# Optimization experiments

Hardware: AMD Instinct MI355X
Metric: run time of the kernel (lower is better)

The kernel has to match this reference:

```python
import jax, jax.numpy as jnp
import numpy as np

N = 50000      # nodes
E = 400000     # edges (before self-loops)
IN = 256       # in_dim
H = 4          # heads in layer 1
C = 64         # h_dim (per-head channels, layer 1)
OUT = 16       # out_dim (layer 2, 1 head)
NEG_SLOPE = 0.2


def gatv2_layer(x, src, dst, Wl, bl, Wr, br, att, bias, heads, ch, concat, num_nodes):
    # x: [N, F]; src/dst: [E']; Wl/Wr: [F, heads*ch]; att: [heads, ch]
    xl = (x @ Wl + bl).reshape(num_nodes, heads, ch)  # source transform
    xr = (x @ Wr + br).reshape(num_nodes, heads, ch)  # target transform
    m = xl[src] + xr[dst]                              # [E', H, C] gather
    e = jnp.sum(jax.nn.leaky_relu(m, NEG_SLOPE) * att, axis=-1)  # [E', H]
    # segment softmax over incoming edges of each dst node (self-loops ensure non-empty)
    emax = jax.ops.segment_max(e, dst, num_segments=num_nodes)   # [N, H]
    ee = jnp.exp(e - emax[dst])
    denom = jax.ops.segment_sum(ee, dst, num_segments=num_nodes)  # [N, H]
    alpha = ee / (denom[dst] + 1e-16)                              # [E', H]
    out = jax.ops.segment_sum(alpha[..., None] * xl[src], dst, num_segments=num_nodes)  # [N,H,C]
    if concat:
        out = out.reshape(num_nodes, heads * ch)
    else:
        out = out.mean(axis=1)
    return out + bias


def setup_inputs() -> dict:
    key = jax.random.key(0)
    ks = jax.random.split(key, 16)
    s = 0.05
    inp = {
        "x": jax.random.normal(ks[0], (N, IN), jnp.float32),
        "edge_index": jax.random.randint(ks[1], (2, E), 0, N),
        # layer 1 params (in_dim -> heads*h_dim)
        "Wl1": jax.random.normal(ks[2], (IN, H * C), jnp.float32) * s,
        "bl1": jnp.zeros((H * C,), jnp.float32),
        "Wr1": jax.random.normal(ks[3], (IN, H * C), jnp.float32) * s,
        "br1": jnp.zeros((H * C,), jnp.float32),
        "att1": jax.random.normal(ks[4], (H, C), jnp.float32) * s,
        "bias1": jnp.zeros((H * C,), jnp.float32),
        # layer 2 params (heads*h_dim -> out_dim, 1 head)
        "Wl2": jax.random.normal(ks[5], (H * C, OUT), jnp.float32) * s,
        "bl2": jnp.zeros((OUT,), jnp.float32),
        "Wr2": jax.random.normal(ks[6], (H * C, OUT), jnp.float32) * s,
        "br2": jnp.zeros((OUT,), jnp.float32),
        "att2": jax.random.normal(ks[7], (1, OUT), jnp.float32) * s,
        "bias2": jnp.zeros((OUT,), jnp.float32),
    }
    return inp


def reference(x, edge_index, Wl1, bl1, Wr1, br1, att1, bias1, Wl2, bl2, Wr2, br2, att2, bias2):
    # add self loops (PyG GATv2Conv default add_self_loops=True)
    loop = jnp.arange(N, dtype=edge_index.dtype)
    src = jnp.concatenate([edge_index[0], loop])
    dst = jnp.concatenate([edge_index[1], loop])
    h = gatv2_layer(x, src, dst, Wl1, bl1, Wr1, br1, att1, bias1, H, C, True, N)
    h = jnp.tanh(h)
    o = gatv2_layer(h, src, dst, Wl2, bl2, Wr2, br2, att2, bias2, 1, OUT, False, N)
    return o, jax.nn.log_softmax(o, axis=1)
```

## Files before the change

### kernel.cpp

```cpp
#include <hip/hip_runtime.h>

typedef __bf16 bfv8 __attribute__((ext_vector_type(8)));
typedef float f32x4 __attribute__((ext_vector_type(4)));
typedef short shortv8 __attribute__((ext_vector_type(8)));

__device__ __forceinline__ float b2f(unsigned short u) {
  unsigned int v = ((unsigned int)u) << 16;
  float f;
  __builtin_memcpy(&f, &v, 4);
  return f;
}
__device__ __forceinline__ unsigned short f2b(float f) {
  unsigned int u;
  __builtin_memcpy(&u, &f, 4);
  u += 0x7fffu + ((u >> 16) & 1u);
  return (unsigned short)(u >> 16);
}

__global__ void probe_kernel(const unsigned short* __restrict__ x, int* __restrict__ flag) {
  int lane = threadIdx.x;
  int cnt = 0;
  for (int i = lane; i < 4096; i += 64) {
    unsigned int e = (x[i] >> 7) & 0xffu;
    if (e >= 0x86u) cnt++;
  }
#pragma unroll
  for (int off = 1; off < 64; off <<= 1) cnt += __shfl_xor(cnt, off, 64);
  if (lane == 0) *flag = (cnt > 100) ? 1 : 0;
}

__global__ __launch_bounds__(256) void conv_x_kernel(const void* __restrict__ x,
                                                     unsigned short* __restrict__ dst,
                                                     const int* __restrict__ flagp, int n) {
  int i = (blockIdx.x * 256 + threadIdx.x) * 4;
  if (i >= n) return;
  if (*flagp) {
    float4 f = *reinterpret_cast<const float4*>((const float*)x + i);
    ushort4 o;
    o.x = f2b(f.x); o.y = f2b(f.y); o.z = f2b(f.z); o.w = f2b(f.w);
    *reinterpret_cast<ushort4*>(dst + i) = o;
  } else {
    *reinterpret_cast<ushort4*>(dst + i) =
        *reinterpret_cast<const ushort4*>((const unsigned short*)x + i);
  }
}

#define P_TOT 140352
__global__ __launch_bounds__(256) void conv_params_kernel(
    const void* p0, const void* p1, const void* p2, const void* p3,
    const void* p4, const void* p5, const void* p6, const void* p7,
    const void* p8, const void* p9, const void* p10, const void* p11,
    unsigned short* __restrict__ dst, const int* __restrict__ flagp) {
  int i = blockIdx.x * 256 + threadIdx.x;
  if (i >= P_TOT) return;
  const int offs[13] = {0, 65536, 65792, 131328, 131584, 131840, 132096,
                        136192, 136208, 140304, 140320, 140336, P_TOT};
  const void* ptrs[12] = {p0, p1, p2, p3, p4, p5, p6, p7, p8, p9, p10, p11};
  int flag = *flagp;
  int t = 0;
  while (i >= offs[t + 1]) t++;
  int local = i - offs[t];
  unsigned short v;
  if (flag) v = f2b(((const float*)ptrs[t])[local]);
  else v = ((const unsigned short*)ptrs[t])[local];
  dst[i] = v;
}

__global__ __launch_bounds__(256) void transpose_w_kernel(
    const unsigned short* __restrict__ Pc,
    unsigned short* __restrict__ WT1, unsigned short* __restrict__ WT2) {
  int idx = blockIdx.x * 256 + threadIdx.x;
  if (idx < 512 * 256) {
    int n = idx >> 8, k = idx & 255;
    WT1[idx] = (n < 256) ? Pc[0 + k * 256 + n]
                         : Pc[65792 + k * 256 + (n - 256)];
  } else {
    int j = idx - 512 * 256;
    if (j < 32 * 256) {
      int n = j >> 8, k = j & 255;
      WT2[j] = (n < 16) ? Pc[132096 + k * 16 + n]
                        : Pc[136208 + k * 16 + (n - 16)];
    }
  }
}

__global__ __launch_bounds__(256) void gemm1_kernel(
    const unsigned short* __restrict__ X,
    const unsigned short* __restrict__ WT,
    const unsigned short* __restrict__ bl, const unsigned short* __restrict__ br,
    unsigned short* __restrict__ C, int M) {
  __shared__ unsigned short smem[18432];
  const int t = threadIdx.x;
  const int lane = t & 63;
  const int w = t >> 6;
  const int quad = lane >> 4;
  const int l16 = lane & 15;
  const int n_blk = blockIdx.x;
  const int m_base = blockIdx.y * 128 + (w >> 1) * 64;
  const int n_base = n_blk * 128 + (w & 1) * 64;

  const int st_row = t >> 3;
  const int st_seg = t & 7;
  const unsigned short* wt_base =
      WT + ((size_t)(n_blk * 128 + st_row)) * 256 + st_seg * 8;

  f32x4 acc[4][4];
#pragma unroll
  for (int i = 0; i < 4; i++)
#pragma unroll
    for (int j = 0; j < 4; j++) acc[i][j] = (f32x4){0.f, 0.f, 0.f, 0.f};

  shortv8 st[4];
#pragma unroll
  for (int i = 0; i < 4; i++)
    st[i] = *reinterpret_cast<const shortv8*>(wt_base + (size_t)(32 * i) * 256);
#pragma unroll
  for (int i = 0; i < 4; i++) {
    int row = st_row + 32 * i;
    *reinterpret_cast<shortv8*>(smem + row * 64 + ((st_seg ^ (row & 7)) * 8)) = st[i];
  }
  __syncthreads();

#pragma unroll
  for (int c = 0; c < 4; c++) {
    if (c < 3) {
#pragma unroll
      for (int i = 0; i < 4; i++)
        st[i] = *reinterpret_cast<const shortv8*>(wt_base + (size_t)(32 * i) * 256 +
                                                  (c + 1) * 64);
    }
    const unsigned short* bb = smem + (c & 1) * 8192;
#pragma unroll
    for (int sub = 0; sub < 2; sub++) {
      bfv8 a[4], b[4];
      int seg_r = sub * 4 + quad;
#pragma unroll
      for (int i = 0; i < 4; i++) {
        int row = m_base + 16 * i + l16;
        if (row >= M) row = M - 1;
        a[i] = *reinterpret_cast<const bfv8*>(X + (size_t)row * 256 + c * 64 + sub * 32 +
                                              quad * 8);
      }
#pragma unroll
      for (int j = 0; j < 4; j++) {
        int col = (w & 1) * 64 + 16 * j + l16;
        b[j] = *reinterpret_cast<const bfv8*>(bb + col * 64 + ((seg_r ^ (col & 7)) * 8));
      }
#pragma unroll
      for (int i = 0; i < 4; i++)
#pragma unroll
        for (int j = 0; j < 4; j++)
          acc[i][j] = __builtin_amdgcn_mfma_f32_16x16x32_bf16(a[i], b[j], acc[i][j], 0, 0, 0);
    }
    if (c < 3) {
      int buf = (c + 1) & 1;
#pragma unroll
      for (int i = 0; i < 4; i++) {
        int row = st_row + 32 * i;
        *reinterpret_cast<shortv8*>(smem + buf * 8192 + row * 64 +
                                    ((st_seg ^ (row & 7)) * 8)) = st[i];
      }
      __syncthreads();
    }
  }

  __syncthreads();
  unsigned short* lt = smem + w * 4608;
#pragma unroll
  for (int j = 0; j < 4; j++) {
    int col = n_base + 16 * j + l16;
    float bias = (col < 256) ? b2f(bl[col]) : b2f(br[col - 256]);
#pragma unroll
    for (int i = 0; i < 4; i++)
#pragma unroll
      for (int r = 0; r < 4; r++)
        lt[(16 * i + quad * 4 + r) * 72 + 16 * j + l16] = f2b(acc[i][j][r] + bias);
  }
#pragma unroll
  for (int pass = 0; pass < 8; pass++) {
    int row = pass * 8 + (lane >> 3);
    int colg = (lane & 7) * 8;
    shortv8 v = *reinterpret_cast<const shortv8*>(lt + row * 72 + colg);
    int grow = m_base + row;
    if (grow < M)
      *reinterpret_cast<shortv8*>(C + (size_t)grow * 512 + n_base - (w & 1) * 64 +
                                  (w & 1) * 64 + colg) = v;
  }
}

__global__ __launch_bounds__(256) void gemm2_kernel(
    const unsigned short* __restrict__ H, const unsigned short* __restrict__ WT,
    const unsigned short* __restrict__ bl, const unsigned short* __restrict__ br,
    float* __restrict__ C, int M) {
  const int lane = threadIdx.x & 63;
  const int w = threadIdx.x >> 6;
  const int quad = lane >> 4;
  const int l16 = lane & 15;
  const int m_base = blockIdx.x * 256 + w * 64;

  f32x4 acc[4][2];
#pragma unroll
  for (int i = 0; i < 4; i++)
#pragma unroll
    for (int j = 0; j < 2; j++) acc[i][j] = (f32x4){0.f, 0.f, 0.f, 0.f};

#pragma unroll
  for (int k0 = 0; k0 < 256; k0 += 32) {
    bfv8 a[4], b[2];
#pragma unroll
    for (int i = 0; i < 4; i++) {
      int row = m_base + 16 * i + l16;
      if (row >= M) row = M - 1;
      a[i] = *reinterpret_cast<const bfv8*>(H + (size_t)row * 256 + k0 + quad * 8);
    }
#pragma unroll
    for (int j = 0; j < 2; j++) {
      int col = 16 * j + l16;
      b[j] = *reinterpret_cast<const bfv8*>(WT + (size_t)col * 256 + k0 + quad * 8);
    }
#pragma unroll
    for (int i = 0; i < 4; i++)
#pragma unroll
      for (int j = 0; j < 2; j++)
        acc[i][j] = __builtin_amdgcn_mfma_f32_16x16x32_bf16(a[i], b[j], acc[i][j], 0, 0, 0);
  }

#pragma unroll
  for (int j = 0; j < 2; j++) {
    int col = 16 * j + l16;
    float bias = (j == 0) ? b2f(bl[l16]) : b2f(br[l16]);
#pragma unroll
    for (int i = 0; i < 4; i++) {
#pragma unroll
      for (int r = 0; r < 4; r++) {
        int row = m_base + 16 * i + quad * 4 + r;
        if (row < M) C[(size_t)row * 32 + col] = acc[i][j][r] + bias;
      }
    }
  }
}

__global__ __launch_bounds__(256) void count_kernel(const int* __restrict__ ei, int E, int Nn,
                                                    int* __restrict__ cnt) {
  int i = blockIdx.x * 256 + threadIdx.x;
  int total = E + Nn;
  if (i >= total) return;
  int d = (i < E) ? ei[E + i] : (i - E);
  if ((unsigned)d >= (unsigned)Nn) d = 0;
  atomicAdd(&cnt[d], 1);
}

__global__ __launch_bounds__(1024) void scan1_kernel(const int* __restrict__ cnt,
                                                     int* __restrict__ row_start,
                                                     int* __restrict__ blkTot, int Nn) {
  __shared__ int buf[1024];
  int t = threadIdx.x;
  int i = blockIdx.x * 1024 + t;
  int v = (i < Nn) ? cnt[i] : 0;
  buf[t] = v;
  __syncthreads();
  for (int off = 1; off < 1024; off <<= 1) {
    int x = (t >= off) ? buf[t - off] : 0;
    __syncthreads();
    buf[t] += x;
    __syncthreads();
  }
  if (i < Nn) row_start[i] = buf[t] - v;
  if (t == 1023) blkTot[blockIdx.x] = buf[1023];
}

__global__ __launch_bounds__(64) void scan2_kernel(const int* __restrict__ blkTot,
                                                   int* __restrict__ blkOff, int nb,
                                                   int* __restrict__ row_start, int Nn,
                                                   int total) {
  int lane = threadIdx.x;
  int v = (lane < nb) ? blkTot[lane] : 0;
  int s = v;
#pragma unroll
  for (int off = 1; off < 64; off <<= 1) {
    int u = __shfl_up(s, off, 64);
    if (lane >= off) s += u;
  }
  if (lane < nb) blkOff[lane] = s - v;
  if (lane == 0) row_start[Nn] = total;
}

__global__ __launch_bounds__(1024) void scan3_kernel(int* __restrict__ row_start,
                                                     int* __restrict__ cursor,
                                                     const int* __restrict__ blkOff, int Nn) {
  int i = blockIdx.x * 1024 + threadIdx.x;
  if (i < Nn) {
    int val = row_start[i] + blkOff[blockIdx.x];
    row_start[i] = val;
    cursor[i] = val;
  }
}

__global__ __launch_bounds__(256) void fill_kernel(const int* __restrict__ ei, int E, int Nn,
                                                   int* __restrict__ cursor,
                                                   int* __restrict__ csr_src) {
  int i = blockIdx.x * 256 + threadIdx.x;
  int total = E + Nn;
  if (i >= total) return;
  int s, d;
  if (i < E) { s = ei[i]; d = ei[E + i]; } else { s = i - E; d = i - E; }
  if ((unsigned)d >= (unsigned)Nn) d = 0;
  if ((unsigned)s >= (unsigned)Nn) s = 0;
  int pos = atomicAdd(&cursor[d], 1);
  if ((unsigned)pos < (unsigned)total) csr_src[pos] = s;
}

__global__ __launch_bounds__(256) void agg1_kernel(
    const unsigned short* __restrict__ C1,
    const unsigned short* __restrict__ att1,
    const unsigned short* __restrict__ bias1,
    const int* __restrict__ row_start, const int* __restrict__ csr_src,
    unsigned short* __restrict__ H1,
    int Nn, int Etot) {
  int wid = blockIdx.x * 4 + (threadIdx.x >> 6);
  if (wid >= Nn) return;
  int lane = threadIdx.x & 63;
  int c0 = lane * 4;

  ushort4 a4 = *reinterpret_cast<const ushort4*>(att1 + c0);
  float at0 = b2f(a4.x), at1 = b2f(a4.y), at2 = b2f(a4.z), at3 = b2f(a4.w);
  ushort4 r4 = *reinterpret_cast<const ushort4*>(C1 + (size_t)wid * 512 + 256 + c0);
  float xr0 = b2f(r4.x), xr1 = b2f(r4.y), xr2 = b2f(r4.z), xr3 = b2f(r4.w);

  float denom = 0.f, a0 = 0.f, a1 = 0.f, a2 = 0.f, a3 = 0.f;
  int beg = row_start[wid], end = row_start[wid + 1];
  if (beg < 0) beg = 0;
  if (end < beg || end - beg > Etot) end = beg;
  int n = end - beg;

  ushort4 cur0 = make_ushort4(0, 0, 0, 0), cur1 = cur0;
  if (n > 0) {
    int s = csr_src[beg];
    if ((unsigned)s >= (unsigned)Nn) s = 0;
    cur0 = *reinterpret_cast<const ushort4*>(C1 + (size_t)s * 512 + c0);
  }
  if (n > 1) {
    int s = csr_src[beg + 1];
    if ((unsigned)s >= (unsigned)Nn) s = 0;
    cur1 = *reinterpret_cast<const ushort4*>(C1 + (size_t)s * 512 + c0);
  }

#define AGG1_BODY(XV)                                                        \
  {                                                                          \
    float xl0 = b2f(XV.x), xl1 = b2f(XV.y), xl2 = b2f(XV.z), xl3 = b2f(XV.w); \
    float m0 = xl0 + xr0, m1 = xl1 + xr1, m2 = xl2 + xr2, m3 = xl3 + xr3;    \
    float l0 = m0 > 0.f ? m0 : 0.2f * m0;                                    \
    float l1 = m1 > 0.f ? m1 : 0.2f * m1;                                    \
    float l2 = m2 > 0.f ? m2 : 0.2f * m2;                                    \
    float l3 = m3 > 0.f ? m3 : 0.2f * m3;                                    \
    float part = l0 * at0 + l1 * at1 + l2 * at2 + l3 * at3;                  \
    part += __shfl_xor(part, 1, 64);                                         \
    part += __shfl_xor(part, 2, 64);                                         \
    part += __shfl_xor(part, 4, 64);                                         \
    part += __shfl_xor(part, 8, 64);                                         \
    part = fminf(fmaxf(part, -60.f), 60.f);                                  \
    float wgt = __expf(part);                                                \
    denom += wgt;                                                            \
    a0 += wgt * xl0; a1 += wgt * xl1; a2 += wgt * xl2; a3 += wgt * xl3;      \
  }

  int i = 0;
  for (; i + 2 <= n; i += 2) {
    ushort4 nxt0 = cur0, nxt1 = cur1;
    int q0 = beg + i + 2, q1 = beg + i + 3;
    if (q0 < end) {
      int s = csr_src[q0];
      if ((unsigned)s >= (unsigned)Nn) s = 0;
      nxt0 = *reinterpret_cast<const ushort4*>(C1 + (size_t)s * 512 + c0);
    }
    if (q1 < end) {
      int s = csr_src[q1];
      if ((unsigned)s >= (unsigned)Nn) s = 0;
      nxt1 = *reinterpret_cast<const ushort4*>(C1 + (size_t)s * 512 + c0);
    }
    AGG1_BODY(cur0);
    AGG1_BODY(cur1);
    cur0 = nxt0;
    cur1 = nxt1;
  }
  if (i < n) AGG1_BODY(cur0);
#undef AGG1_BODY

  float inv = 1.f / (denom + 1e-16f);
  ushort4 b4 = *reinterpret_cast<const ushort4*>(bias1 + c0);
  float h0 = tanhf(a0 * inv + b2f(b4.x));
  float h1 = tanhf(a1 * inv + b2f(b4.y));
  float h2 = tanhf(a2 * inv + b2f(b4.z));
  float h3 = tanhf(a3 * inv + b2f(b4.w));
  if (!(h0 == h0)) h0 = 0.f;
  if (!(h1 == h1)) h1 = 0.f;
  if (!(h2 == h2)) h2 = 0.f;
  if (!(h3 == h3)) h3 = 0.f;
  ushort4 o4;
  o4.x = f2b(h0); o4.y = f2b(h1); o4.z = f2b(h2); o4.w = f2b(h3);
  *reinterpret_cast<ushort4*>(H1 + (size_t)wid * 256 + c0) = o4;
}

__global__ __launch_bounds__(256) void agg2_kernel(
    const float* __restrict__ C2,
    const unsigned short* __restrict__ att2,
    const unsigned short* __restrict__ bias2,
    const int* __restrict__ row_start, const int* __restrict__ csr_src,
    float* __restrict__ out,
    int Nn, int Etot) {
  int wid = blockIdx.x * 4 + (threadIdx.x >> 6);
  if (wid >= Nn) return;
  int lane = threadIdx.x & 63;
  int g = lane >> 4;
  int c = lane & 15;

  float att = b2f(att2[c]);
  float xr = C2[(size_t)wid * 32 + 16 + c];
  float denom = 0.f, acc = 0.f;
  int beg = row_start[wid], end = row_start[wid + 1];
  if (beg < 0) beg = 0;
  if (end < beg || end - beg > Etot) end = beg;

  int p = beg + g;
  float xl_cur = 0.f;
  if (p < end) {
    int s = csr_src[p];
    if ((unsigned)s >= (unsigned)Nn) s = 0;
    xl_cur = C2[(size_t)s * 32 + c];
  }
  while (p < end) {
    int pn = p + 4;
    float xl_nxt = 0.f;
    if (pn < end) {
      int s = csr_src[pn];
      if ((unsigned)s >= (unsigned)Nn) s = 0;
      xl_nxt = C2[(size_t)s * 32 + c];
    }
    float mm = xl_cur + xr;
    float lr = mm > 0.f ? mm : 0.2f * mm;
    float part = lr * att;
    part += __shfl_xor(part, 1, 64);
    part += __shfl_xor(part, 2, 64);
    part += __shfl_xor(part, 4, 64);
    part += __shfl_xor(part, 8, 64);
    part = fminf(fmaxf(part, -60.f), 60.f);
    float wgt = __expf(part);
    denom += wgt;
    acc += wgt * xl_cur;
    xl_cur = xl_nxt;
    p = pn;
  }
  denom += __shfl_xor(denom, 16, 64);
  denom += __shfl_xor(denom, 32, 64);
  acc += __shfl_xor(acc, 16, 64);
  acc += __shfl_xor(acc, 32, 64);

  float o = acc / (denom + 1e-16f) + b2f(bias2[c]);
  if (!(o == o)) o = 0.f;
  float mx = o;
  mx = fmaxf(mx, __shfl_xor(mx, 1, 64));
  mx = fmaxf(mx, __shfl_xor(mx, 2, 64));
  mx = fmaxf(mx, __shfl_xor(mx, 4, 64));
  mx = fmaxf(mx, __shfl_xor(mx, 8, 64));
  float ex = expf(o - mx);
  float se = ex;
  se += __shfl_xor(se, 1, 64);
  se += __shfl_xor(se, 2, 64);
  se += __shfl_xor(se, 4, 64);
  se += __shfl_xor(se, 8, 64);
  float ls = logf(se);
  if (lane < 16) {
    out[(size_t)wid * 16 + c] = o;
    out[(size_t)Nn * 16 + (size_t)wid * 16 + c] = o - mx - ls;
  }
}

extern "C" void kernel_launch(void* const* d_in, const int* in_sizes, int n_in,
                              void* d_out, int out_size, void* d_ws, size_t ws_size,
                              hipStream_t stream) {
  const void* x_raw = d_in[0];
  const int* ei     = (const int*)d_in[1];

  const int M = in_sizes[0] / 256;
  const int E = in_sizes[1] / 2;
  const int TOT = E + M;
  const int NX = M * 256;

  char* ws = (char*)d_ws;
  size_t off = 0;
  auto alloc = [&](size_t bytes) -> void* {
    void* p = ws + off;
    off = (off + bytes + 255) & ~(size_t)255;
    return p;
  };
  int*            flag   = (int*)alloc(4);
  unsigned short* Pc     = (unsigned short*)alloc((size_t)P_TOT * 2);
  unsigned short* Xc     = (unsigned short*)alloc((size_t)NX * 2);
  unsigned short* WT1    = (unsigned short*)alloc((size_t)512 * 256 * 2);
  unsigned short* WT2    = (unsigned short*)alloc((size_t)32 * 256 * 2);
  int*            cnt    = (int*)alloc((size_t)M * 4);
  int*            cursor = (int*)alloc((size_t)M * 4);
  int*            row_start = (int*)alloc((size_t)(M + 1) * 4);
  int*            csr_src   = (int*)alloc((size_t)TOT * 4);
  int*            blkTot = (int*)alloc(64 * 4);
  int*            blkOff = (int*)alloc(64 * 4);
  float*          C2     = (float*)alloc((size_t)M * 32 * 4);
  unsigned short* C1     = (unsigned short*)alloc((size_t)M * 512 * 2);
  const size_t need = off;
  (void)n_in;
  unsigned short* H1 = Xc;

  if (ws_size < need) {
    hipMemsetAsync(d_out, 0, (size_t)out_size * 4, stream);
    return;
  }

  unsigned short* bl1c   = Pc + 65536;
  unsigned short* br1c   = Pc + 131328;
  unsigned short* att1c  = Pc + 131584;
  unsigned short* bias1c = Pc + 131840;
  unsigned short* bl2c   = Pc + 136192;
  unsigned short* br2c   = Pc + 140304;
  unsigned short* att2c  = Pc + 140320;
  unsigned short* bias2c = Pc + 140336;

  hipMemsetAsync(cnt, 0, (size_t)M * 4, stream);

  probe_kernel<<<1, 64, 0, stream>>>((const unsigned short*)x_raw, flag);
  conv_x_kernel<<<(NX / 4 + 255) / 256, 256, 0, stream>>>(x_raw, Xc, flag, NX);
  conv_params_kernel<<<(P_TOT + 255) / 256, 256, 0, stream>>>(
      d_in[2], d_in[3], d_in[4], d_in[5], d_in[6], d_in[7], d_in[8], d_in[9],
      d_in[10], d_in[11], d_in[12], d_in[13], Pc, flag);

  transpose_w_kernel<<<(512 * 256 + 32 * 256 + 255) / 256, 256, 0, stream>>>(Pc, WT1, WT2);

  dim3 g1(4, (M + 127) / 128);
  gemm1_kernel<<<g1, 256, 0, stream>>>(Xc, WT1, bl1c, br1c, C1, M);

  count_kernel<<<(TOT + 255) / 256, 256, 0, stream>>>(ei, E, M, cnt);
  int nb = (M + 1023) / 1024;
  scan1_kernel<<<nb, 1024, 0, stream>>>(cnt, row_start, blkTot, M);
  scan2_kernel<<<1, 64, 0, stream>>>(blkTot, blkOff, nb, row_start, M, TOT);
  scan3_kernel<<<nb, 1024, 0, stream>>>(row_start, cursor, blkOff, M);
  fill_kernel<<<(TOT + 255) / 256, 256, 0, stream>>>(ei, E, M, cursor, csr_src);

  agg1_kernel<<<(M + 3) / 4, 256, 0, stream>>>(C1, att1c, bias1c, row_start, csr_src,
                                               H1, M, TOT);

  gemm2_kernel<<<(M + 255) / 256, 256, 0, stream>>>(H1, WT2, bl2c, br2c, C2, M);

  agg2_kernel<<<(M + 3) / 4, 256, 0, stream>>>(C2, att2c, bias2c, row_start, csr_src,
                                               (float*)d_out, M, TOT);
}
```

Baseline: 316.0 us.

## Process multiple edges per wavefront in GAT aggregation kernels with wider vector loads

The layer-1 aggregation now splits each wavefront into two halves that handle two edges at once, each lane loading 8 bf16 channels with a 16-byte load. The layer-2 aggregation handles 16 edges per iteration with float4 loads per lane. Both kernels combine partial sums with cross-lane shuffles at the end. The aim is more independent gathers in flight and fewer loop iterations per node, at the cost of dropping the explicit software prefetch, wasting lanes on short neighbour lists, and replacing tanhf with an exp-based formula.

```diff
diff --git a/kernel.cpp b/kernel.cpp
--- a/kernel.cpp
+++ b/kernel.cpp
@@ -3,6 +3,7 @@
 typedef __bf16 bfv8 __attribute__((ext_vector_type(8)));
 typedef float f32x4 __attribute__((ext_vector_type(4)));
 typedef short shortv8 __attribute__((ext_vector_type(8)));
+typedef unsigned short usv8 __attribute__((ext_vector_type(8)));
 
 __device__ __forceinline__ float b2f(unsigned short u) {
   unsigned int v = ((unsigned int)u) << 16;
@@ -183,8 +184,7 @@
     shortv8 v = *reinterpret_cast<const shortv8*>(lt + row * 72 + colg);
     int grow = m_base + row;
     if (grow < M)
-      *reinterpret_cast<shortv8*>(C + (size_t)grow * 512 + n_base - (w & 1) * 64 +
-                                  (w & 1) * 64 + colg) = v;
+      *reinterpret_cast<shortv8*>(C + (size_t)grow * 512 + n_base + colg) = v;
   }
 }
 
@@ -320,85 +320,66 @@
   int wid = blockIdx.x * 4 + (threadIdx.x >> 6);
   if (wid >= Nn) return;
   int lane = threadIdx.x & 63;
-  int c0 = lane * 4;
-
-  ushort4 a4 = *reinterpret_cast<const ushort4*>(att1 + c0);
-  float at0 = b2f(a4.x), at1 = b2f(a4.y), at2 = b2f(a4.z), at3 = b2f(a4.w);
-  ushort4 r4 = *reinterpret_cast<const ushort4*>(C1 + (size_t)wid * 512 + 256 + c0);
-  float xr0 = b2f(r4.x), xr1 = b2f(r4.y), xr2 = b2f(r4.z), xr3 = b2f(r4.w);
-
-  float denom = 0.f, a0 = 0.f, a1 = 0.f, a2 = 0.f, a3 = 0.f;
+  int half = lane >> 5;
+  int c0 = (lane & 31) * 8;
+
+  float at[8], xr[8];
+  {
+    usv8 a8 = *reinterpret_cast<const usv8*>(att1 + c0);
+    usv8 r8 = *reinterpret_cast<const usv8*>(C1 + (size_t)wid * 512 + 256 + c0);
+#pragma unroll
+    for (int k = 0; k < 8; k++) { at[k] = b2f(a8[k]); xr[k] = b2f(r8[k]); }
+  }
+
+  float denom = 0.f;
+  float acc[8] = {0.f, 0.f, 0.f, 0.f, 0.f, 0.f, 0.f, 0.f};
   int beg = row_start[wid], end = row_start[wid + 1];
   if (beg < 0) beg = 0;
   if (end < beg || end - beg > Etot) end = beg;
-  int n = end - beg;
-
-  ushort4 cur0 = make_ushort4(0, 0, 0, 0), cur1 = cur0;
-  if (n > 0) {
-    int s = csr_src[beg];
+
+#pragma unroll 2
+  for (int i = beg; i < end; i += 2) {
+    int p = i + half;
+    bool valid = p < end;
+    int pc = valid ? p : i;
+    int s = csr_src[pc];
     if ((unsigned)s >= (unsigned)Nn) s = 0;
-    cur0 = *reinterpret_cast<const ushort4*>(C1 + (size_t)s * 512 + c0);
-  }
-  if (n > 1) {
-    int s = csr_src[beg + 1];
-    if ((unsigned)s >= (unsigned)Nn) s = 0;
-    cur1 = *reinterpret_cast<const ushort4*>(C1 + (size_t)s * 512 + c0);
-  }
-
-#define AGG1_BODY(XV)                                                        \
-  {                                                                          \
-    float xl0 = b2f(XV.x), xl1 = b2f(XV.y), xl2 = b2f(XV.z), xl3 = b2f(XV.w); \
-    float m0 = xl0 + xr0, m1 = xl1 + xr1, m2 = xl2 + xr2, m3 = xl3 + xr3;    \
-    float l0 = m0 > 0.f ? m0 : 0.2f * m0;                                    \
-    float l1 = m1 > 0.f ? m1 : 0.2f * m1;                                    \
-    float l2 = m2 > 0.f ? m2 : 0.2f * m2;                                    \
-    float l3 = m3 > 0.f ? m3 : 0.2f * m3;                                    \
-    float part = l0 * at0 + l1 * at1 + l2 * at2 + l3 * at3;                  \
-    part += __shfl_xor(part, 1, 64);                                         \
-    part += __shfl_xor(part, 2, 64);                                         \
-    part += __shfl_xor(part, 4, 64);                                         \
-    part += __shfl_xor(part, 8, 64);                                         \
-    part = fminf(fmaxf(part, -60.f), 60.f);                                  \
-    float wgt = __expf(part);                                                \
-    denom += wgt;                                                            \
-    a0 += wgt * xl0; a1 += wgt * xl1; a2 += wgt * xl2; a3 += wgt * xl3;      \
-  }
-
-  int i = 0;
-  for (; i + 2 <= n; i += 2) {
-    ushort4 nxt0 = cur0, nxt1 = cur1;
-    int q0 = beg + i + 2, q1 = beg + i + 3;
-    if (q0 < end) {
-      int s = csr_src[q0];
-      if ((unsigned)s >= (unsigned)Nn) s = 0;
-      nxt0 = *reinterpret_cast<const ushort4*>(C1 + (size_t)s * 512 + c0);
-    }
-    if (q1 < end) {
-      int s = csr_src[q1];
-      if ((unsigned)s >= (unsigned)Nn) s = 0;
-      nxt1 = *reinterpret_cast<const ushort4*>(C1 + (size_t)s * 512 + c0);
-    }
-    AGG1_BODY(cur0);
-    AGG1_BODY(cur1);
-    cur0 = nxt0;
-    cur1 = nxt1;
-  }
-  if (i < n) AGG1_BODY(cur0);
-#undef AGG1_BODY
-
-  float inv = 1.f / (denom + 1e-16f);
-  ushort4 b4 = *reinterpret_cast<const ushort4*>(bias1 + c0);
-  float h0 = tanhf(a0 * inv + b2f(b4.x));
-  float h1 = tanhf(a1 * inv + b2f(b4.y));
-  float h2 = tanhf(a2 * inv + b2f(b4.z));
-  float h3 = tanhf(a3 * inv + b2f(b4.w));
-  if (!(h0 == h0)) h0 = 0.f;
-  if (!(h1 == h1)) h1 = 0.f;
-  if (!(h2 == h2)) h2 = 0.f;
-  if (!(h3 == h3)) h3 = 0.f;
-  ushort4 o4;
-  o4.x = f2b(h0); o4.y = f2b(h1); o4.z = f2b(h2); o4.w = f2b(h3);
-  *reinterpret_cast<ushort4*>(H1 + (size_t)wid * 256 + c0) = o4;
+    usv8 row = *reinterpret_cast<const usv8*>(C1 + (size_t)s * 512 + c0);
+    float xl[8], dot = 0.f;
+#pragma unroll
+    for (int k = 0; k < 8; k++) {
+      xl[k] = b2f(row[k]);
+      float m = xl[k] + xr[k];
+      float l = fmaxf(m, 0.2f * m);
+      dot = fmaf(l, at[k], dot);
+    }
+    dot += __shfl_xor(dot, 1, 64);
+    dot += __shfl_xor(dot, 2, 64);
+    dot += __shfl_xor(dot, 4, 64);
+    dot = fminf(fmaxf(dot, -60.f), 60.f);
+    float wgt = valid ? __expf(dot) : 0.f;
+    denom += wgt;
+#pragma unroll
+    for (int k = 0; k < 8; k++) acc[k] = fmaf(wgt, xl[k], acc[k]);
+  }
+  denom += __shfl_xor(denom, 32, 64);
+#pragma unroll
+  for (int k = 0; k < 8; k++) acc[k] += __shfl_xor(acc[k], 32, 64);
+
+  if (half == 0) {
+    float inv = 1.f / (denom + 1e-16f);
+    usv8 b8 = *reinterpret_cast<const usv8*>(bias1 + c0);
+    usv8 o8;
+#pragma unroll
+    for (int k = 0; k < 8; k++) {
+      float x = acc[k] * inv + b2f(b8[k]);
+      float e2 = __expf(2.f * x);
+      float th = (e2 - 1.f) / (e2 + 1.f);
+      if (!(th == th)) th = 0.f;
+      o8[k] = f2b(th);
+    }
+    *reinterpret_cast<usv8*>(H1 + (size_t)wid * 256 + c0) = o8;
+  }
 }
 
 __global__ __launch_bounds__(256) void agg2_kernel(
@@ -411,67 +392,76 @@
   int wid = blockIdx.x * 4 + (threadIdx.x >> 6);
   if (wid >= Nn) return;
   int lane = threadIdx.x & 63;
-  int g = lane >> 4;
-  int c = lane & 15;
-
-  float att = b2f(att2[c]);
-  float xr = C2[(size_t)wid * 32 + 16 + c];
-  float denom = 0.f, acc = 0.f;
+  int eslot = lane >> 2;
+  int cg = (lane & 3) * 4;
+
+  float at[4], xr[4];
+  {
+    ushort4 a4 = *reinterpret_cast<const ushort4*>(att2 + cg);
+    at[0] = b2f(a4.x); at[1] = b2f(a4.y); at[2] = b2f(a4.z); at[3] = b2f(a4.w);
+    float4 r4 = *reinterpret_cast<const float4*>(C2 + (size_t)wid * 32 + 16 + cg);
+    xr[0] = r4.x; xr[1] = r4.y; xr[2] = r4.z; xr[3] = r4.w;
+  }
+
+  float denom = 0.f;
+  float acc[4] = {0.f, 0.f, 0.f, 0.f};
   int beg = row_start[wid], end = row_start[wid + 1];
   if (beg < 0) beg = 0;
   if (end < beg || end - beg > Etot) end = beg;
 
-  int p = beg + g;
-  float xl_cur = 0.f;
-  if (p < end) {
-    int s = csr_src[p];
+  for (int i = beg; i < end; i += 16) {
+    int p = i + eslot;
+    bool valid = p < end;
+    int pc = valid ? p : i;
+    int s = csr_src[pc];
     if ((unsigned)s >= (unsigned)Nn) s = 0;
-    xl_cur = C2[(size_t)s * 32 + c];
-  }
-  while (p < end) {
-    int pn = p + 4;
-    float xl_nxt = 0.f;
-    if (pn < end) {
-      int s = csr_src[pn];
-      if ((unsigned)s >= (unsigned)Nn) s = 0;
-      xl_nxt = C2[(size_t)s * 32 + c];
-    }
-    float mm = xl_cur + xr;
-    float lr = mm > 0.f ? mm : 0.2f * mm;
-    float part = lr * att;
-    part += __shfl_xor(part, 1, 64);
-    part += __shfl_xor(part, 2, 64);
-    part += __shfl_xor(part, 4, 64);
-    part += __shfl_xor(part, 8, 64);
-    part = fminf(fmaxf(part, -60.f), 60.f);
-    float wgt = __expf(part);
+    float4 x4 = *reinterpret_cast<const float4*>(C2 + (size_t)s * 32 + cg);
+    float xl[4] = {x4.x, x4.y, x4.z, x4.w};
+    float dot = 0.f;
+#pragma unroll
+    for (int k = 0; k < 4; k++) {
+      float m = xl[k] + xr[k];
+      float l = fmaxf(m, 0.2f * m);
+      dot = fmaf(l, at[k], dot);
+    }
+    dot += __shfl_xor(dot, 1, 64);
+    dot += __shfl_xor(dot, 2, 64);
+    dot = fminf(fmaxf(dot, -60.f), 60.f);
+    float wgt = valid ? __expf(dot) : 0.f;
     denom += wgt;
-    acc += wgt * xl_cur;
-    xl_cur = xl_nxt;
-    p = pn;
-  }
-  denom += __shfl_xor(denom, 16, 64);
-  denom += __shfl_xor(denom, 32, 64);
-  acc += __shfl_xor(acc, 16, 64);
-  acc += __shfl_xor(acc, 32, 64);
-
-  float o = acc / (denom + 1e-16f) + b2f(bias2[c]);
-  if (!(o == o)) o = 0.f;
-  float mx = o;
+#pragma unroll
+    for (int k = 0; k < 4; k++) acc[k] = fmaf(wgt, xl[k], acc[k]);
+  }
+#pragma unroll
+  for (int off = 4; off <= 32; off <<= 1) {
+    denom += __shfl_xor(denom, off, 64);
+#pragma unroll
+    for (int k = 0; k < 4; k++) acc[k] += __shfl_xor(acc[k], off, 64);
+  }
+
+  float inv = 1.f / (denom + 1e-16f);
+  ushort4 b4 = *reinterpret_cast<const ushort4*>(bias2 + cg);
+  float bb[4] = {b2f(b4.x), b2f(b4.y), b2f(b4.z), b2f(b4.w)};
+  float o[4];
+#pragma unroll
+  for (int k = 0; k < 4; k++) {
+    o[k] = acc[k] * inv + bb[k];
+    if (!(o[k] == o[k])) o[k] = 0.f;
+  }
+  float mx = fmaxf(fmaxf(o[0], o[1]), fmaxf(o[2], o[3]));
   mx = fmaxf(mx, __shfl_xor(mx, 1, 64));
   mx = fmaxf(mx, __shfl_xor(mx, 2, 64));
-  mx = fmaxf(mx, __shfl_xor(mx, 4, 64));
-  mx = fmaxf(mx, __shfl_xor(mx, 8, 64));
-  float ex = expf(o - mx);
-  float se = ex;
+  float se = 0.f;
+#pragma unroll
+  for (int k = 0; k < 4; k++) se += __expf(o[k] - mx);
   se += __shfl_xor(se, 1, 64);
   se += __shfl_xor(se, 2, 64);
-  se += __shfl_xor(se, 4, 64);
-  se += __shfl_xor(se, 8, 64);
   float ls = logf(se);
-  if (lane < 16) {
-    out[(size_t)wid * 16 + c] = o;
-    out[(size_t)Nn * 16 + (size_t)wid * 16 + c] = o - mx - ls;
+  if (lane < 4) {
+    float4 vo = {o[0], o[1], o[2], o[3]};
+    float4 vl = {o[0] - mx - ls, o[1] - mx - ls, o[2] - mx - ls, o[3] - mx - ls};
+    *reinterpret_cast<float4*>(out + (size_t)wid * 16 + cg) = vo;
+    *reinterpret_cast<float4*>(out + (size_t)Nn * 16 + (size_t)wid * 16 + cg) = vl;
   }
 }
 
```

Measured after the change: 301.6 us. -4.6%, faster.
